# Optimization experiments

Hardware: AMD Instinct MI355X
Metric: run time of the kernel (lower is better)

## Reference

```python
import jax, jax.numpy as jnp
import numpy as np

F8 = jnp.float8_e4m3fn
F8_MAX = 448.0  # torch.finfo(float8_e4m3fn).max


def _quantize(t):
    """Per-tensor FP8 e4m3 quantization with amax scaling (TensorCoreFP8Layout.quantize
    with scale='recalculate'). Returns (fp8_data, float32_scale)."""
    scale = jnp.max(jnp.abs(t)) / F8_MAX
    q = jnp.clip(t * (1.0 / scale), -F8_MAX, F8_MAX).astype(F8)
    return q, scale.astype(jnp.float32)


def setup_inputs() -> dict:
    key = jax.random.key(0)
    k1, k2, k3 = jax.random.split(key, 3)
    B, S, D_IN, D_OUT = 4, 4096, 4096, 4096
    x = jax.random.normal(k1, (B, S, D_IN), dtype=jnp.float32)
    weight = jax.random.normal(k2, (D_OUT, D_IN), dtype=jnp.float32) * 0.02
    bias = jax.random.normal(k3, (D_OUT,), dtype=jnp.float32) * 0.02
    return {"x": x, "weight": weight, "bias": bias}


def reference(x, weight, bias):
    # Quantize weight (done once at load time in the original) and activation
    # (dynamic per-tensor quantization) to fp8 e4m3 with amax scales.
    wq, sw = _quantize(weight)
    xq, sx = _quantize(x)
    # Scaled matmul: fp8 values are dequantized into the GEMM accumulator dtype;
    # the combined scale sx*sw is applied to the output (fused dequant-matmul).
    out = jnp.einsum(
        "bsd,od->bso", xq.astype(jnp.float32), wq.astype(jnp.float32)
    ) * (sx * sw)
    return out + bias
```

## Files before the change

kernel.cpp:

```cpp
#include <hip/hip_runtime.h>

typedef float floatx4 __attribute__((ext_vector_type(4)));
typedef long longx2 __attribute__((ext_vector_type(2)));

#define F8_MAX 448.0f
#define BM 128
#define BN 128
#define BK 64

__global__ void amax_kernel(const float* __restrict__ x, int n4,
                            unsigned* __restrict__ out) {
  const float4* __restrict__ x4 = (const float4*)x;
  float m = 0.0f;
  int stride = gridDim.x * blockDim.x;
  for (int i = blockIdx.x * blockDim.x + threadIdx.x; i < n4; i += stride) {
    float4 v = x4[i];
    m = fmaxf(m, fmaxf(fmaxf(fabsf(v.x), fabsf(v.y)),
                       fmaxf(fabsf(v.z), fabsf(v.w))));
  }
  for (int off = 32; off > 0; off >>= 1)
    m = fmaxf(m, __shfl_down(m, off, 64));
  __shared__ float wmax[4];
  int wave = threadIdx.x >> 6;
  if ((threadIdx.x & 63) == 0) wmax[wave] = m;
  __syncthreads();
  if (threadIdx.x == 0) {
    float bm = fmaxf(fmaxf(wmax[0], wmax[1]), fmaxf(wmax[2], wmax[3]));
    atomicMax(out, __float_as_uint(bm));
  }
}

__global__ void quant_kernel(const float* __restrict__ x,
                             unsigned char* __restrict__ q, int n8,
                             const unsigned* __restrict__ amax_bits) {
  float amax = __uint_as_float(*amax_bits);
  float scale = amax / F8_MAX;
  float inv = 1.0f / scale;
  const float4* __restrict__ x4 = (const float4*)x;
  uint2* __restrict__ q8 = (uint2*)q;
  int stride = gridDim.x * blockDim.x;
  for (int i = blockIdx.x * blockDim.x + threadIdx.x; i < n8; i += stride) {
    float4 a = x4[2 * i];
    float4 b = x4[2 * i + 1];
    float c0 = fminf(fmaxf(a.x * inv, -F8_MAX), F8_MAX);
    float c1 = fminf(fmaxf(a.y * inv, -F8_MAX), F8_MAX);
    float c2 = fminf(fmaxf(a.z * inv, -F8_MAX), F8_MAX);
    float c3 = fminf(fmaxf(a.w * inv, -F8_MAX), F8_MAX);
    float c4 = fminf(fmaxf(b.x * inv, -F8_MAX), F8_MAX);
    float c5 = fminf(fmaxf(b.y * inv, -F8_MAX), F8_MAX);
    float c6 = fminf(fmaxf(b.z * inv, -F8_MAX), F8_MAX);
    float c7 = fminf(fmaxf(b.w * inv, -F8_MAX), F8_MAX);
    int lo = __builtin_amdgcn_cvt_pk_fp8_f32(c0, c1, 0, false);
    lo = __builtin_amdgcn_cvt_pk_fp8_f32(c2, c3, lo, true);
    int hi = __builtin_amdgcn_cvt_pk_fp8_f32(c4, c5, 0, false);
    hi = __builtin_amdgcn_cvt_pk_fp8_f32(c6, c7, hi, true);
    uint2 r;
    r.x = (unsigned)lo;
    r.y = (unsigned)hi;
    q8[i] = r;
  }
}

__device__ inline void async_copy16(const unsigned char* g, unsigned char* l) {
  __builtin_amdgcn_global_load_lds(
      (const __attribute__((address_space(1))) void*)g,
      (__attribute__((address_space(3))) void*)l, 16, 0, 0);
}

__global__ void __launch_bounds__(256) gemm_fp8(
    const unsigned char* __restrict__ Xq, const unsigned char* __restrict__ Wq,
    const float* __restrict__ bias, const unsigned* __restrict__ scales,
    float* __restrict__ C, int M, int N, int K) {
  __shared__ __align__(16) unsigned char As[BM * BK];
  __shared__ __align__(16) unsigned char Bs[BN * BK];

  const int tid = threadIdx.x;
  const int wave = tid >> 6;
  const int lane = tid & 63;
  const int quad = lane >> 4;
  const int l16 = lane & 15;
  const int wm = wave & 1;
  const int wn = wave >> 1;

  const int baseM = blockIdx.y * BM;
  const int baseN = blockIdx.x * BN;

  floatx4 acc[4][4];
#pragma unroll
  for (int i = 0; i < 4; i++)
#pragma unroll
    for (int j = 0; j < 4; j++) acc[i][j] = {0.f, 0.f, 0.f, 0.f};

  const int srow = tid >> 2;
  const int skoff = ((tid & 3) ^ (srow & 3)) * 16;
  const unsigned char* gA0 = Xq + (size_t)(baseM + srow) * K + skoff;
  const unsigned char* gA1 = gA0 + (size_t)64 * K;
  const unsigned char* gB0 = Wq + (size_t)(baseN + srow) * K + skoff;
  const unsigned char* gB1 = gB0 + (size_t)64 * K;
  unsigned char* lA0 = As + wave * 1024;
  unsigned char* lA1 = As + 4096 + wave * 1024;
  unsigned char* lB0 = Bs + wave * 1024;
  unsigned char* lB1 = Bs + 4096 + wave * 1024;

  const int aOff = (wm * 64 + l16) * BK + ((quad ^ (l16 & 3)) * 16);
  const int bOff = (wn * 64 + l16) * BK + ((quad ^ (l16 & 3)) * 16);

  for (int kt = 0; kt < K; kt += BK) {
    async_copy16(gA0 + kt, lA0);
    async_copy16(gA1 + kt, lA1);
    async_copy16(gB0 + kt, lB0);
    async_copy16(gB1 + kt, lB1);
    __syncthreads();

    longx2 a[4], b[4];
#pragma unroll
    for (int i = 0; i < 4; i++)
      a[i] = *(const longx2*)(As + aOff + i * 16 * BK);
#pragma unroll
    for (int i = 0; i < 4; i++)
      b[i] = *(const longx2*)(Bs + bOff + i * 16 * BK);
#pragma unroll
    for (int mi = 0; mi < 4; mi++)
#pragma unroll
      for (int ni = 0; ni < 4; ni++)
        acc[mi][ni] = __builtin_amdgcn_mfma_f32_16x16x32_fp8_fp8(
            a[mi].x, b[ni].x, acc[mi][ni], 0, 0, 0);
#pragma unroll
    for (int mi = 0; mi < 4; mi++)
#pragma unroll
      for (int ni = 0; ni < 4; ni++)
        acc[mi][ni] = __builtin_amdgcn_mfma_f32_16x16x32_fp8_fp8(
            a[mi].y, b[ni].y, acc[mi][ni], 0, 0, 0);

    __syncthreads();
  }

  const float s = (__uint_as_float(scales[0]) / F8_MAX) *
                  (__uint_as_float(scales[1]) / F8_MAX);
#pragma unroll
  for (int ni = 0; ni < 4; ni++) {
    const int gn = baseN + wn * 64 + ni * 16 + l16;
    const float bv = bias[gn];
#pragma unroll
    for (int mi = 0; mi < 4; mi++) {
      const int gm = baseM + wm * 64 + mi * 16 + quad * 4;
      float* outp = C + (size_t)gm * N + gn;
#pragma unroll
      for (int r = 0; r < 4; r++) outp[(size_t)r * N] = acc[mi][ni][r] * s + bv;
    }
  }
}

extern "C" void kernel_launch(void* const* d_in, const int* in_sizes, int n_in,
                              void* d_out, int out_size, void* d_ws,
                              size_t ws_size, hipStream_t stream) {
  const float* x = (const float*)d_in[0];
  const float* w = (const float*)d_in[1];
  const float* bias = (const float*)d_in[2];
  float* out = (float*)d_out;

  const int N = in_sizes[2];
  const int K = in_sizes[1] / N;
  const int M = in_sizes[0] / K;

  unsigned* scales = (unsigned*)d_ws;
  unsigned char* xq = (unsigned char*)d_ws + 256;
  unsigned char* wq = xq + (size_t)M * K;

  hipMemsetAsync(d_ws, 0, 256, stream);
  amax_kernel<<<4096, 256, 0, stream>>>(x, (M * K) / 4, scales + 0);
  amax_kernel<<<1024, 256, 0, stream>>>(w, (N * K) / 4, scales + 1);
  quant_kernel<<<4096, 256, 0, stream>>>(x, xq, (M * K) / 8, scales + 0);
  quant_kernel<<<1024, 256, 0, stream>>>(w, wq, (N * K) / 8, scales + 1);

  dim3 grid(N / BN, M / BM);
  gemm_fp8<<<grid, 256, 0, stream>>>(xq, wq, bias, scales, out, M, N, K);
}
```

Before: 1.041 ms.

## Enlarge GEMM tiles with 4-stage async LDS pipeline and merge prep kernels

```diff
diff --git a/kernel.cpp b/kernel.cpp
--- a/kernel.cpp
+++ b/kernel.cpp
@@ -1,20 +1,27 @@
 #include <hip/hip_runtime.h>
 
 typedef float floatx4 __attribute__((ext_vector_type(4)));
-typedef long longx2 __attribute__((ext_vector_type(2)));
 
 #define F8_MAX 448.0f
-#define BM 128
-#define BN 128
+#define BM 256
+#define BN 256
 #define BK 64
-
-__global__ void amax_kernel(const float* __restrict__ x, int n4,
-                            unsigned* __restrict__ out) {
-  const float4* __restrict__ x4 = (const float4*)x;
+#define TILE_A (BM * BK)
+#define TILE_B (BN * BK)
+
+__global__ void amax2_kernel(const float* __restrict__ x, int n4x,
+                             const float* __restrict__ w, int n4w,
+                             unsigned* __restrict__ out, int nbx) {
+  const bool isX = (int)blockIdx.x < nbx;
+  const float4* __restrict__ src = (const float4*)(isX ? x : w);
+  const int n4 = isX ? n4x : n4w;
+  const int bid = isX ? (int)blockIdx.x : (int)blockIdx.x - nbx;
+  const int nb = isX ? nbx : (int)gridDim.x - nbx;
   float m = 0.0f;
-  int stride = gridDim.x * blockDim.x;
-  for (int i = blockIdx.x * blockDim.x + threadIdx.x; i < n4; i += stride) {
-    float4 v = x4[i];
+  const int stride = nb * blockDim.x;
+#pragma unroll 4
+  for (int i = bid * blockDim.x + threadIdx.x; i < n4; i += stride) {
+    float4 v = src[i];
     m = fmaxf(m, fmaxf(fmaxf(fabsf(v.x), fabsf(v.y)),
                        fmaxf(fabsf(v.z), fabsf(v.w))));
   }
@@ -26,38 +33,35 @@
   __syncthreads();
   if (threadIdx.x == 0) {
     float bm = fmaxf(fmaxf(wmax[0], wmax[1]), fmaxf(wmax[2], wmax[3]));
-    atomicMax(out, __float_as_uint(bm));
-  }
-}
-
-__global__ void quant_kernel(const float* __restrict__ x,
-                             unsigned char* __restrict__ q, int n8,
-                             const unsigned* __restrict__ amax_bits) {
-  float amax = __uint_as_float(*amax_bits);
-  float scale = amax / F8_MAX;
-  float inv = 1.0f / scale;
-  const float4* __restrict__ x4 = (const float4*)x;
-  uint2* __restrict__ q8 = (uint2*)q;
-  int stride = gridDim.x * blockDim.x;
-  for (int i = blockIdx.x * blockDim.x + threadIdx.x; i < n8; i += stride) {
-    float4 a = x4[2 * i];
-    float4 b = x4[2 * i + 1];
-    float c0 = fminf(fmaxf(a.x * inv, -F8_MAX), F8_MAX);
-    float c1 = fminf(fmaxf(a.y * inv, -F8_MAX), F8_MAX);
-    float c2 = fminf(fmaxf(a.z * inv, -F8_MAX), F8_MAX);
-    float c3 = fminf(fmaxf(a.w * inv, -F8_MAX), F8_MAX);
-    float c4 = fminf(fmaxf(b.x * inv, -F8_MAX), F8_MAX);
-    float c5 = fminf(fmaxf(b.y * inv, -F8_MAX), F8_MAX);
-    float c6 = fminf(fmaxf(b.z * inv, -F8_MAX), F8_MAX);
-    float c7 = fminf(fmaxf(b.w * inv, -F8_MAX), F8_MAX);
-    int lo = __builtin_amdgcn_cvt_pk_fp8_f32(c0, c1, 0, false);
-    lo = __builtin_amdgcn_cvt_pk_fp8_f32(c2, c3, lo, true);
-    int hi = __builtin_amdgcn_cvt_pk_fp8_f32(c4, c5, 0, false);
-    hi = __builtin_amdgcn_cvt_pk_fp8_f32(c6, c7, hi, true);
-    uint2 r;
-    r.x = (unsigned)lo;
-    r.y = (unsigned)hi;
-    q8[i] = r;
+    atomicMax(out + (isX ? 0 : 1), __float_as_uint(bm));
+  }
+}
+
+__global__ void quant2_kernel(const float* __restrict__ x,
+                              unsigned char* __restrict__ xq, int n4x,
+                              const float* __restrict__ w,
+                              unsigned char* __restrict__ wq, int n4w,
+                              const unsigned* __restrict__ amax_bits, int nbx) {
+  const bool isX = (int)blockIdx.x < nbx;
+  const float amax = __uint_as_float(amax_bits[isX ? 0 : 1]);
+  const float scale = amax / F8_MAX;
+  const float inv = 1.0f / scale;
+  const float4* __restrict__ src = (const float4*)(isX ? x : w);
+  unsigned* __restrict__ dst = (unsigned*)(isX ? xq : wq);
+  const int n4 = isX ? n4x : n4w;
+  const int bid = isX ? (int)blockIdx.x : (int)blockIdx.x - nbx;
+  const int nb = isX ? nbx : (int)gridDim.x - nbx;
+  const int stride = nb * blockDim.x;
+#pragma unroll 2
+  for (int i = bid * blockDim.x + threadIdx.x; i < n4; i += stride) {
+    float4 v = src[i];
+    float c0 = fminf(fmaxf(v.x * inv, -F8_MAX), F8_MAX);
+    float c1 = fminf(fmaxf(v.y * inv, -F8_MAX), F8_MAX);
+    float c2 = fminf(fmaxf(v.z * inv, -F8_MAX), F8_MAX);
+    float c3 = fminf(fmaxf(v.w * inv, -F8_MAX), F8_MAX);
+    int p = __builtin_amdgcn_cvt_pk_fp8_f32(c0, c1, 0, false);
+    p = __builtin_amdgcn_cvt_pk_fp8_f32(c2, c3, p, true);
+    dst[i] = (unsigned)p;
   }
 }
 
@@ -67,73 +71,108 @@
       (__attribute__((address_space(3))) void*)l, 16, 0, 0);
 }
 
-__global__ void __launch_bounds__(256) gemm_fp8(
+__global__ void __launch_bounds__(512) gemm_fp8(
     const unsigned char* __restrict__ Xq, const unsigned char* __restrict__ Wq,
     const float* __restrict__ bias, const unsigned* __restrict__ scales,
     float* __restrict__ C, int M, int N, int K) {
-  __shared__ __align__(16) unsigned char As[BM * BK];
-  __shared__ __align__(16) unsigned char Bs[BN * BK];
+  __shared__ __align__(16) unsigned char As[4 * TILE_A];
+  __shared__ __align__(16) unsigned char Bs[4 * TILE_B];
 
   const int tid = threadIdx.x;
   const int wave = tid >> 6;
   const int lane = tid & 63;
   const int quad = lane >> 4;
   const int l16 = lane & 15;
-  const int wm = wave & 1;
-  const int wn = wave >> 1;
+  const int wm = wave >> 2;
+  const int wn = wave & 3;
 
   const int baseM = blockIdx.y * BM;
   const int baseN = blockIdx.x * BN;
 
-  floatx4 acc[4][4];
-#pragma unroll
-  for (int i = 0; i < 4; i++)
+  floatx4 acc[8][4];
+#pragma unroll
+  for (int i = 0; i < 8; i++)
 #pragma unroll
     for (int j = 0; j < 4; j++) acc[i][j] = {0.f, 0.f, 0.f, 0.f};
 
-  const int srow = tid >> 2;
-  const int skoff = ((tid & 3) ^ (srow & 3)) * 16;
-  const unsigned char* gA0 = Xq + (size_t)(baseM + srow) * K + skoff;
-  const unsigned char* gA1 = gA0 + (size_t)64 * K;
-  const unsigned char* gB0 = Wq + (size_t)(baseN + srow) * K + skoff;
-  const unsigned char* gB1 = gB0 + (size_t)64 * K;
-  unsigned char* lA0 = As + wave * 1024;
-  unsigned char* lA1 = As + 4096 + wave * 1024;
-  unsigned char* lB0 = Bs + wave * 1024;
-  unsigned char* lB1 = Bs + 4096 + wave * 1024;
-
-  const int aOff = (wm * 64 + l16) * BK + ((quad ^ (l16 & 3)) * 16);
-  const int bOff = (wn * 64 + l16) * BK + ((quad ^ (l16 & 3)) * 16);
-
-  for (int kt = 0; kt < K; kt += BK) {
-    async_copy16(gA0 + kt, lA0);
-    async_copy16(gA1 + kt, lA1);
-    async_copy16(gB0 + kt, lB0);
-    async_copy16(gB1 + kt, lB1);
-    __syncthreads();
-
-    longx2 a[4], b[4];
-#pragma unroll
-    for (int i = 0; i < 4; i++)
-      a[i] = *(const longx2*)(As + aOff + i * 16 * BK);
-#pragma unroll
-    for (int i = 0; i < 4; i++)
-      b[i] = *(const longx2*)(Bs + bOff + i * 16 * BK);
-#pragma unroll
-    for (int mi = 0; mi < 4; mi++)
-#pragma unroll
-      for (int ni = 0; ni < 4; ni++)
-        acc[mi][ni] = __builtin_amdgcn_mfma_f32_16x16x32_fp8_fp8(
-            a[mi].x, b[ni].x, acc[mi][ni], 0, 0, 0);
-#pragma unroll
-    for (int mi = 0; mi < 4; mi++)
-#pragma unroll
-      for (int ni = 0; ni < 4; ni++)
-        acc[mi][ni] = __builtin_amdgcn_mfma_f32_16x16x32_fp8_fp8(
-            a[mi].y, b[ni].y, acc[mi][ni], 0, 0, 0);
-
-    __syncthreads();
-  }
+  const int sr = tid >> 2;
+  const int sj = (tid & 3) ^ ((tid >> 3) & 3);
+  const unsigned char* gA0 = Xq + (size_t)(baseM + sr) * K + sj * 16;
+  const unsigned char* gA1 = gA0 + (size_t)128 * K;
+  const unsigned char* gB0 = Wq + (size_t)(baseN + sr) * K + sj * 16;
+  const unsigned char* gB1 = gB0 + (size_t)128 * K;
+  const int stOff = wave * 1024;
+
+  const int swl = (l16 >> 1) & 3;
+  const int q1 = quad >> 1, q0 = quad & 1;
+  const int cs0 = ((q1 ^ swl) * 16) + q0 * 8;
+  const int cs1 = (((2 + q1) ^ swl) * 16) + q0 * 8;
+  const int aBase = (wm * 128 + l16) * BK;
+  const int bBase = (wn * 64 + l16) * BK;
+
+  const int nt = K / BK;
+
+  async_copy16(gA0, As + stOff);
+  async_copy16(gA1, As + 8192 + stOff);
+  async_copy16(gB0, Bs + stOff);
+  async_copy16(gB1, Bs + 8192 + stOff);
+  if (nt > 1) {
+    async_copy16(gA0 + BK, As + TILE_A + stOff);
+    async_copy16(gA1 + BK, As + TILE_A + 8192 + stOff);
+    async_copy16(gB0 + BK, Bs + TILE_B + stOff);
+    async_copy16(gB1 + BK, Bs + TILE_B + 8192 + stOff);
+    asm volatile("s_waitcnt vmcnt(4)" ::: "memory");
+  } else {
+    asm volatile("s_waitcnt vmcnt(0)" ::: "memory");
+  }
+  __builtin_amdgcn_s_barrier();
+
+  long a[4], b[4];
+
+#define PHASE(HH, CS, DOB, STAGE)                                              \
+  {                                                                            \
+    _Pragma("unroll") for (int mi = 0; mi < 4; ++mi) a[mi] =                   \
+        *(const long*)(Ab + aBase + ((HH)*4 + mi) * 1024 + (CS));              \
+    if (DOB) {                                                                 \
+      _Pragma("unroll") for (int ni = 0; ni < 4; ++ni) b[ni] =                 \
+          *(const long*)(Bb + bBase + ni * 1024 + (CS));                       \
+    }                                                                          \
+    STAGE                                                                      \
+    __builtin_amdgcn_s_barrier();                                              \
+    asm volatile("s_waitcnt lgkmcnt(0)" ::: "memory");                         \
+    __builtin_amdgcn_s_setprio(1);                                             \
+    _Pragma("unroll") for (int mi = 0; mi < 4; ++mi) {                         \
+      _Pragma("unroll") for (int ni = 0; ni < 4; ++ni) acc[(HH)*4 + mi][ni] =  \
+          __builtin_amdgcn_mfma_f32_16x16x32_fp8_fp8(                          \
+              a[mi], b[ni], acc[(HH)*4 + mi][ni], 0, 0, 0);                    \
+    }                                                                          \
+    __builtin_amdgcn_s_setprio(0);                                             \
+  }
+
+#pragma unroll 1
+  for (int t = 0; t < nt; ++t) {
+    const unsigned char* Ab = As + (t & 3) * TILE_A;
+    const unsigned char* Bb = Bs + (t & 3) * TILE_B;
+    const bool stg = (t + 2 < nt);
+    const int bo2a = ((t + 2) & 3) * TILE_A;
+    const int bo2b = ((t + 2) & 3) * TILE_B;
+    const size_t k2 = (size_t)(t + 2) * BK;
+
+    PHASE(0, cs0, 1, { if (stg) async_copy16(gA0 + k2, As + bo2a + stOff); })
+    __builtin_amdgcn_s_barrier();
+    PHASE(1, cs0, 0, { if (stg) async_copy16(gA1 + k2, As + bo2a + 8192 + stOff); })
+    __builtin_amdgcn_s_barrier();
+    PHASE(0, cs1, 1, { if (stg) async_copy16(gB0 + k2, Bs + bo2b + stOff); })
+    __builtin_amdgcn_s_barrier();
+    PHASE(1, cs1, 0, { if (stg) async_copy16(gB1 + k2, Bs + bo2b + 8192 + stOff); })
+    if (stg) {
+      asm volatile("s_waitcnt vmcnt(4)" ::: "memory");
+    } else {
+      asm volatile("s_waitcnt vmcnt(0)" ::: "memory");
+    }
+    __builtin_amdgcn_s_barrier();
+  }
+#undef PHASE
 
   const float s = (__uint_as_float(scales[0]) / F8_MAX) *
                   (__uint_as_float(scales[1]) / F8_MAX);
@@ -142,8 +181,8 @@
     const int gn = baseN + wn * 64 + ni * 16 + l16;
     const float bv = bias[gn];
 #pragma unroll
-    for (int mi = 0; mi < 4; mi++) {
-      const int gm = baseM + wm * 64 + mi * 16 + quad * 4;
+    for (int mi = 0; mi < 8; mi++) {
+      const int gm = baseM + wm * 128 + mi * 16 + quad * 4;
       float* outp = C + (size_t)gm * N + gn;
 #pragma unroll
       for (int r = 0; r < 4; r++) outp[(size_t)r * N] = acc[mi][ni][r] * s + bv;
@@ -167,12 +206,15 @@
   unsigned char* xq = (unsigned char*)d_ws + 256;
   unsigned char* wq = xq + (size_t)M * K;
 
+  const int NBX = 4096;
+  const int NBW = 1024;
+
   hipMemsetAsync(d_ws, 0, 256, stream);
-  amax_kernel<<<4096, 256, 0, stream>>>(x, (M * K) / 4, scales + 0);
-  amax_kernel<<<1024, 256, 0, stream>>>(w, (N * K) / 4, scales + 1);
-  quant_kernel<<<4096, 256, 0, stream>>>(x, xq, (M * K) / 8, scales + 0);
-  quant_kernel<<<1024, 256, 0, stream>>>(w, wq, (N * K) / 8, scales + 1);
+  amax2_kernel<<<NBX + NBW, 256, 0, stream>>>(x, (M * K) / 4, w, (N * K) / 4,
+                                              scales, NBX);
+  quant2_kernel<<<NBX + NBW, 256, 0, stream>>>(x, xq, (M * K) / 4, w, wq,
+                                               (N * K) / 4, scales, NBX);
 
   dim3 grid(N / BN, M / BM);
-  gemm_fp8<<<grid, 256, 0, stream>>>(xq, wq, bias, scales, out, M, N, K);
-}
+  gemm_fp8<<<grid, 512, 0, stream>>>(xq, wq, bias, scales, out, M, N, K);
+}
```

Result: faster. 996.3 us (-4.3%).
